# Performance work log

Measured on AMD Instinct MI355X. Metric: run time of the kernel, lower is better.

The kernel has to match this reference:

```python
import jax, jax.numpy as jnp
import numpy as np


def setup_inputs() -> dict:
    key = jax.random.key(0)
    ks = jax.random.split(key, 8)
    B, N = 4, 256
    E, C, H = 64, 128, 256
    return {
        "edge_features": jax.random.normal(ks[0], (B, E, N, N), dtype=jnp.float32),
        "node_features": jax.random.normal(ks[1], (B, C, N), dtype=jnp.float32),
        "W1": jax.random.normal(ks[2], (H, E + 2 * C), dtype=jnp.float32) * 0.05,
        "b1": jax.random.normal(ks[3], (H,), dtype=jnp.float32) * 0.05,
        "W2": jax.random.normal(ks[4], (H, H), dtype=jnp.float32) * 0.05,
        "b2": jax.random.normal(ks[5], (H,), dtype=jnp.float32) * 0.05,
        "W3": jax.random.normal(ks[6], (1, H), dtype=jnp.float32) * 0.05,
        "b3": jax.random.normal(ks[7], (1,), dtype=jnp.float32) * 0.05,
    }


def reference(edge_features, node_features, W1, b1, W2, b2, W3, b3):
    B, C, N = node_features.shape
    # node_addon_row: [B, C, N, N] broadcast along last dim; col along dim 2
    row = jnp.broadcast_to(node_features[:, :, :, None], (B, C, N, N))
    col = jnp.broadcast_to(node_features[:, :, None, :], (B, C, N, N))
    x = jnp.concatenate([edge_features, row, col], axis=1)  # [B, E+2C, N, N]
    # 1x1 conv == channel matmul
    x = jax.nn.relu(jnp.einsum('bcnm,oc->bonm', x, W1) + b1[None, :, None, None])
    x = jax.nn.relu(jnp.einsum('bcnm,oc->bonm', x, W2) + b2[None, :, None, None])
    x = jnp.einsum('bcnm,oc->bonm', x, W3) + b3[None, :, None, None]  # [B,1,N,N]
    return x[:, 0, :, :]
```

## Files before the change

kernel.cpp:

```cpp
#include <hip/hip_runtime.h>
#include <stdint.h>

typedef __bf16 bf16x8 __attribute__((ext_vector_type(8)));
typedef __bf16 bf16x4v __attribute__((ext_vector_type(4)));
typedef float  f32x16 __attribute__((ext_vector_type(16)));
typedef float  f32x4t __attribute__((ext_vector_type(4)));
typedef unsigned int u32x2 __attribute__((ext_vector_type(2)));

#define WS_W1S 0
#define WS_W2S 32768
#define WS_R   163840
#define WS_CT  1212416

__global__ void prep_weights(const float* __restrict__ W1, const float* __restrict__ W2,
                             __bf16* __restrict__ w1s, __bf16* __restrict__ w2s) {
    int t = blockIdx.x * 256 + threadIdx.x;
    int chunk = t >> 6, lane = t & 63;
    if (chunk < 128) {
        int wid = chunk >> 5, ks = (chunk >> 1) & 15, mb = chunk & 1;
        int o = wid * 64 + mb * 32 + (lane & 31);
        int k = ks * 16 + (lane >> 5) * 8;
        const float* src = W2 + o * 256 + k;
        __bf16* dst = w2s + chunk * 512 + lane * 8;
#pragma unroll
        for (int j = 0; j < 8; ++j) dst[j] = (__bf16)src[j];
    } else if (chunk < 160) {
        int c1 = chunk - 128;
        int wid = c1 >> 3, ks = (c1 >> 1) & 3, mb = c1 & 1;
        int o = wid * 64 + mb * 32 + (lane & 31);
        int k = ks * 16 + (lane >> 5) * 8;
        const float* src = W1 + o * 320 + k;
        __bf16* dst = w1s + c1 * 512 + lane * 8;
#pragma unroll
        for (int j = 0; j < 8; ++j) dst[j] = (__bf16)src[j];
    }
}

__global__ __launch_bounds__(256) void prep_rc(
    const float* __restrict__ W1, const float* __restrict__ b1,
    const float* __restrict__ node, float* __restrict__ Rt,
    __bf16* __restrict__ Ctb) {
    __shared__ float nds[128 * 16];
    const int b = blockIdx.x >> 4, j0 = (blockIdx.x & 15) * 16;
    const int o = threadIdx.x;
    {
        int c = threadIdx.x >> 1, jh = (threadIdx.x & 1) * 8;
        const float* src = node + b * 32768 + c * 256 + j0 + jh;
        *(float4*)&nds[c * 16 + jh] = *(const float4*)src;
        *(float4*)&nds[c * 16 + jh + 4] = *(const float4*)(src + 4);
    }
    __syncthreads();
    float aR[16], aC[16];
#pragma unroll
    for (int j = 0; j < 16; ++j) { aR[j] = 0.f; aC[j] = 0.f; }
    const float* wr = W1 + o * 320 + 64;
    const float* wc = W1 + o * 320 + 192;
    for (int c4 = 0; c4 < 32; ++c4) {
        float4 wrv = *(const float4*)(wr + c4 * 4);
        float4 wcv = *(const float4*)(wc + c4 * 4);
        const float* wrp = (const float*)&wrv;
        const float* wcp = (const float*)&wcv;
#pragma unroll
        for (int r = 0; r < 4; ++r) {
            const f32x4t* nrow = (const f32x4t*)&nds[(c4 * 4 + r) * 16];
            f32x4t n0 = nrow[0], n1 = nrow[1], n2 = nrow[2], n3 = nrow[3];
#pragma unroll
            for (int q = 0; q < 4; ++q) {
                aR[q]      = fmaf(wrp[r], n0[q], aR[q]);
                aR[q + 4]  = fmaf(wrp[r], n1[q], aR[q + 4]);
                aR[q + 8]  = fmaf(wrp[r], n2[q], aR[q + 8]);
                aR[q + 12] = fmaf(wrp[r], n3[q], aR[q + 12]);
                aC[q]      = fmaf(wcp[r], n0[q], aC[q]);
                aC[q + 4]  = fmaf(wcp[r], n1[q], aC[q + 4]);
                aC[q + 8]  = fmaf(wcp[r], n2[q], aC[q + 8]);
                aC[q + 12] = fmaf(wcp[r], n3[q], aC[q + 12]);
            }
        }
    }
    float bb = b1[o];
#pragma unroll
    for (int j = 0; j < 16; ++j) {
        int idx = ((b * 256 + j0 + j) << 8) + o;
        Rt[idx] = aR[j] + bb;
        Ctb[idx] = (__bf16)aC[j];
    }
}

__device__ inline void zero_acc(f32x16 acc[2][2]) {
#pragma unroll
    for (int i = 0; i < 2; ++i)
#pragma unroll
        for (int j = 0; j < 2; ++j)
#pragma unroll
            for (int k = 0; k < 16; ++k) acc[i][j][k] = 0.f;
}

__global__ __launch_bounds__(256, 2) void fused_main(
    const float* __restrict__ edge, const __bf16* __restrict__ w1s,
    const __bf16* __restrict__ w2s, const float* __restrict__ Rt,
    const __bf16* __restrict__ Ctb, const float* __restrict__ b2,
    const float* __restrict__ W3, const float* __restrict__ b3,
    float* __restrict__ out) {
    __shared__ unsigned int lds_e[64 * 33];
    __shared__ unsigned int lds_h1[64 * 140];
    __shared__ float lds_p[64 * 9];
    __shared__ float lds_c[512];

    const int tid = threadIdx.x;
    const int wid = tid >> 6;
    const int lane = tid & 63;
    const int p31 = lane & 31;
    const int hi = lane >> 5;
    const int obase = wid * 64;

    const int blk = blockIdx.x;
    const int b   = blk >> 7;
    const int m0  = ((blk >> 5) & 3) << 6;
    const int n0  = (blk & 31) << 3;

    lds_c[tid] = b2[tid];
    lds_c[256 + tid] = W3[tid];

    const float4* eg = (const float4*)edge;
    const int a_ = tid & 15;
    const int epb = tid >> 4;
    float4 pf[4];

#define PREFETCH(nn)                                                        \
    {                                                                       \
        _Pragma("unroll")                                                   \
        for (int r = 0; r < 2; ++r) {                                       \
            int ep = r * 16 + epb;                                          \
            int f4 = (b * 64 + ep * 2) * 16384 + (nn) * 64 + (m0 >> 2) + a_;\
            pf[r * 2]     = eg[f4];                                         \
            pf[r * 2 + 1] = eg[f4 + 16384];                                 \
        }                                                                   \
    }

#define LOAD_Q(bf, q)                                                       \
    {                                                                       \
        _Pragma("unroll")                                                   \
        for (int ksl = 0; ksl < 4; ++ksl)                                   \
            _Pragma("unroll")                                               \
            for (int mb = 0; mb < 2; ++mb)                                  \
                A2q[bf][ksl][mb] = *(const bf16x8*)(w2_s +                  \
                    ((((wid << 4) + (q) * 4 + ksl) << 1) + mb) * 512 + (lane << 3)); \
    }

    PREFETCH(n0);

    bf16x4v CvR[8][2];
#pragma unroll
    for (int mb = 0; mb < 2; ++mb)
#pragma unroll
        for (int rg = 0; rg < 4; ++rg)
#pragma unroll
            for (int nb = 0; nb < 2; ++nb)
                CvR[mb * 4 + rg][nb] = *(const bf16x4v*)(Ctb +
                    ((b * 256 + m0 + nb * 32 + p31) << 8) + obase + mb * 32 + 8 * rg + 4 * hi);

    f32x16 acc[2][2];
    bf16x8 A2q[2][4][2];
    for (int it = 0; it < 8; ++it) {
        const int n = n0 + it;

        uint64_t w1a = (uint64_t)w1s;
        asm volatile("" : "+s"(w1a));
        const __bf16* w1_s = (const __bf16*)w1a;
        uint64_t w2a = (uint64_t)w2s;
        asm volatile("" : "+s"(w2a));
        const __bf16* w2_s = (const __bf16*)w2a;

#pragma unroll
        for (int r = 0; r < 2; ++r) {
            int ep = r * 16 + epb;
            const float* p0 = (const float*)&pf[r * 2];
            const float* p1 = (const float*)&pf[r * 2 + 1];
#pragma unroll
            for (int i = 0; i < 4; ++i) {
                union { __bf16 h[2]; unsigned int u; } t;
                t.h[0] = (__bf16)p0[i];
                t.h[1] = (__bf16)p1[i];
                lds_e[(a_ * 4 + i) * 33 + ep] = t.u;
            }
        }
        bf16x8 A1[2][4];
#pragma unroll
        for (int mb = 0; mb < 2; ++mb)
#pragma unroll
            for (int ks = 0; ks < 4; ++ks)
                A1[mb][ks] = *(const bf16x8*)(w1_s +
                    ((((wid << 2) + ks) << 1) + mb) * 512 + (lane << 3));
        __syncthreads();

        zero_acc(acc);
#pragma unroll
        for (int ks = 0; ks < 4; ++ks) {
            bf16x8 B1[2];
#pragma unroll
            for (int nb = 0; nb < 2; ++nb) {
                union { unsigned int u[4]; bf16x8 v; } bb;
#pragma unroll
                for (int j = 0; j < 4; ++j)
                    bb.u[j] = lds_e[(nb * 32 + p31) * 33 + ks * 8 + hi * 4 + j];
                B1[nb] = bb.v;
            }
#pragma unroll
            for (int mb = 0; mb < 2; ++mb) {
                acc[mb][0] = __builtin_amdgcn_mfma_f32_32x32x16_bf16(A1[mb][ks], B1[0], acc[mb][0], 0, 0, 0);
                acc[mb][1] = __builtin_amdgcn_mfma_f32_32x32x16_bf16(A1[mb][ks], B1[1], acc[mb][1], 0, 0, 0);
            }
        }

        const int nRow = (b * 256 + n) << 8;
#pragma unroll
        for (int mb = 0; mb < 2; ++mb) {
#pragma unroll
            for (int rg = 0; rg < 4; ++rg) {
                int och = obase + mb * 32 + 8 * rg + 4 * hi;
                f32x4t Rv = *(const f32x4t*)(Rt + nRow + och);
#pragma unroll
                for (int nb = 0; nb < 2; ++nb) {
                    int pix = nb * 32 + p31;
                    bf16x4v Cv = CvR[mb * 4 + rg][nb];
                    union { __bf16 h[4]; u32x2 u; } t;
#pragma unroll
                    for (int rr = 0; rr < 4; ++rr) {
                        float v = acc[mb][nb][rg * 4 + rr] + Rv[rr] + (float)Cv[rr];
                        t.h[rr] = (__bf16)fmaxf(v, 0.f);
                    }
                    *(u32x2*)&lds_h1[pix * 140 + (och >> 1)] = t.u;
                }
            }
        }
        LOAD_Q(0, 0);
        if (it < 7) PREFETCH(n + 1);
        __syncthreads();

        zero_acc(acc);
#pragma unroll
        for (int q = 0; q < 4; ++q) {
            if (q < 3) LOAD_Q((q + 1) & 1, q + 1);
#pragma unroll
            for (int ksl = 0; ksl < 4; ++ksl) {
                const int ksg = q * 4 + ksl;
                bf16x8 B2[2];
#pragma unroll
                for (int nb = 0; nb < 2; ++nb)
                    B2[nb] = *(const bf16x8*)&lds_h1[(nb * 32 + p31) * 140 + ksg * 8 + hi * 4];
#pragma unroll
                for (int mb = 0; mb < 2; ++mb) {
                    acc[mb][0] = __builtin_amdgcn_mfma_f32_32x32x16_bf16(A2q[q & 1][ksl][mb], B2[0], acc[mb][0], 0, 0, 0);
                    acc[mb][1] = __builtin_amdgcn_mfma_f32_32x32x16_bf16(A2q[q & 1][ksl][mb], B2[1], acc[mb][1], 0, 0, 0);
                }
            }
        }

        float part0 = 0.f, part1 = 0.f;
#pragma unroll
        for (int mb = 0; mb < 2; ++mb) {
#pragma unroll
            for (int rg = 0; rg < 4; ++rg) {
                int och = obase + mb * 32 + 8 * rg + 4 * hi;
                f32x4t b2v = *(const f32x4t*)&lds_c[och];
                f32x4t w3v = *(const f32x4t*)&lds_c[256 + och];
#pragma unroll
                for (int rr = 0; rr < 4; ++rr) {
                    float h0 = fmaxf(acc[mb][0][rg * 4 + rr] + b2v[rr], 0.f);
                    float h1v = fmaxf(acc[mb][1][rg * 4 + rr] + b2v[rr], 0.f);
                    part0 = fmaf(w3v[rr], h0, part0);
                    part1 = fmaf(w3v[rr], h1v, part1);
                }
            }
        }
        lds_p[(0 * 32 + p31) * 9 + wid * 2 + hi] = part0;
        lds_p[(1 * 32 + p31) * 9 + wid * 2 + hi] = part1;
        __syncthreads();

        if (tid < 64) {
            float s = b3[0];
#pragma unroll
            for (int k = 0; k < 8; ++k) s += lds_p[tid * 9 + k];
            out[((b * 256 + n) << 8) + m0 + tid] = s;
        }
    }
#undef PREFETCH
#undef LOAD_Q
}

extern "C" void kernel_launch(void* const* d_in, const int* in_sizes, int n_in,
                              void* d_out, int out_size, void* d_ws, size_t ws_size,
                              hipStream_t stream) {
    const float* edge = (const float*)d_in[0];
    const float* node = (const float*)d_in[1];
    const float* W1   = (const float*)d_in[2];
    const float* b1   = (const float*)d_in[3];
    const float* W2   = (const float*)d_in[4];
    const float* b2   = (const float*)d_in[5];
    const float* W3   = (const float*)d_in[6];
    const float* b3   = (const float*)d_in[7];
    char* ws = (char*)d_ws;
    __bf16* w1s = (__bf16*)(ws + WS_W1S);
    __bf16* w2s = (__bf16*)(ws + WS_W2S);
    float*  Rt  = (float*)(ws + WS_R);
    __bf16* Ctb = (__bf16*)(ws + WS_CT);

    prep_weights<<<40, 256, 0, stream>>>(W1, W2, w1s, w2s);
    prep_rc<<<64, 256, 0, stream>>>(W1, b1, node, Rt, Ctb);
    fused_main<<<512, 256, 0, stream>>>(edge, w1s, w2s, Rt, Ctb, b2, W3, b3, (float*)d_out);
}
```

Measured before the change: 161.9 us.

## Merge prep kernels, double main grid, raise occupancy, pad LDS, hoist R loads

The two prep kernels are merged into one launch, and the row/col projection is split into finer 4-column blocks so it runs across more workgroups. The main kernel now runs 1024 blocks of 4 rows each instead of 512 blocks of 8, and its launch bounds ask for 3 blocks per CU. The edge LDS tile stride is padded from 33 to 34 so B1 fragments load as 64-bit reads, and the R bias loads are hoisted ahead of the barrier. The cost is a lower register budget per thread, which may cause spills, and the per-block setup is amortised over fewer rows.

```diff
diff --git a/kernel.cpp b/kernel.cpp
--- a/kernel.cpp
+++ b/kernel.cpp
@@ -12,47 +12,44 @@
 #define WS_R   163840
 #define WS_CT  1212416
 
-__global__ void prep_weights(const float* __restrict__ W1, const float* __restrict__ W2,
-                             __bf16* __restrict__ w1s, __bf16* __restrict__ w2s) {
-    int t = blockIdx.x * 256 + threadIdx.x;
-    int chunk = t >> 6, lane = t & 63;
-    if (chunk < 128) {
-        int wid = chunk >> 5, ks = (chunk >> 1) & 15, mb = chunk & 1;
-        int o = wid * 64 + mb * 32 + (lane & 31);
-        int k = ks * 16 + (lane >> 5) * 8;
-        const float* src = W2 + o * 256 + k;
-        __bf16* dst = w2s + chunk * 512 + lane * 8;
-#pragma unroll
-        for (int j = 0; j < 8; ++j) dst[j] = (__bf16)src[j];
-    } else if (chunk < 160) {
-        int c1 = chunk - 128;
-        int wid = c1 >> 3, ks = (c1 >> 1) & 3, mb = c1 & 1;
-        int o = wid * 64 + mb * 32 + (lane & 31);
-        int k = ks * 16 + (lane >> 5) * 8;
-        const float* src = W1 + o * 320 + k;
-        __bf16* dst = w1s + c1 * 512 + lane * 8;
-#pragma unroll
-        for (int j = 0; j < 8; ++j) dst[j] = (__bf16)src[j];
-    }
-}
-
-__global__ __launch_bounds__(256) void prep_rc(
+__global__ __launch_bounds__(256) void prep_all(
     const float* __restrict__ W1, const float* __restrict__ b1,
-    const float* __restrict__ node, float* __restrict__ Rt,
-    __bf16* __restrict__ Ctb) {
-    __shared__ float nds[128 * 16];
-    const int b = blockIdx.x >> 4, j0 = (blockIdx.x & 15) * 16;
+    const float* __restrict__ W2, const float* __restrict__ node,
+    __bf16* __restrict__ w1s, __bf16* __restrict__ w2s,
+    float* __restrict__ Rt, __bf16* __restrict__ Ctb) {
+    __shared__ float nds[128 * 4];
+    const int blk = blockIdx.x;
+    if (blk < 40) {
+        int t = blk * 256 + threadIdx.x;
+        int chunk = t >> 6, lane = t & 63;
+        if (chunk < 128) {
+            int wid = chunk >> 5, ks = (chunk >> 1) & 15, mb = chunk & 1;
+            int o = wid * 64 + mb * 32 + (lane & 31);
+            int k = ks * 16 + (lane >> 5) * 8;
+            const float* src = W2 + o * 256 + k;
+            __bf16* dst = w2s + chunk * 512 + lane * 8;
+#pragma unroll
+            for (int j = 0; j < 8; ++j) dst[j] = (__bf16)src[j];
+        } else if (chunk < 160) {
+            int c1 = chunk - 128;
+            int wid = c1 >> 3, ks = (c1 >> 1) & 3, mb = c1 & 1;
+            int o = wid * 64 + mb * 32 + (lane & 31);
+            int k = ks * 16 + (lane >> 5) * 8;
+            const float* src = W1 + o * 320 + k;
+            __bf16* dst = w1s + c1 * 512 + lane * 8;
+#pragma unroll
+            for (int j = 0; j < 8; ++j) dst[j] = (__bf16)src[j];
+        }
+        return;
+    }
+    const int rcb = blk - 40;
+    const int b = rcb >> 6, j0 = (rcb & 63) << 2;
     const int o = threadIdx.x;
-    {
-        int c = threadIdx.x >> 1, jh = (threadIdx.x & 1) * 8;
-        const float* src = node + b * 32768 + c * 256 + j0 + jh;
-        *(float4*)&nds[c * 16 + jh] = *(const float4*)src;
-        *(float4*)&nds[c * 16 + jh + 4] = *(const float4*)(src + 4);
-    }
+    if (o < 128)
+        *(float4*)&nds[o * 4] = *(const float4*)(node + b * 32768 + o * 256 + j0);
     __syncthreads();
-    float aR[16], aC[16];
-#pragma unroll
-    for (int j = 0; j < 16; ++j) { aR[j] = 0.f; aC[j] = 0.f; }
+    float aR[4] = {0.f, 0.f, 0.f, 0.f};
+    float aC[4] = {0.f, 0.f, 0.f, 0.f};
     const float* wr = W1 + o * 320 + 64;
     const float* wc = W1 + o * 320 + 192;
     for (int c4 = 0; c4 < 32; ++c4) {
@@ -62,24 +59,17 @@
         const float* wcp = (const float*)&wcv;
 #pragma unroll
         for (int r = 0; r < 4; ++r) {
-            const f32x4t* nrow = (const f32x4t*)&nds[(c4 * 4 + r) * 16];
-            f32x4t n0 = nrow[0], n1 = nrow[1], n2 = nrow[2], n3 = nrow[3];
+            f32x4t n4 = *(const f32x4t*)&nds[(c4 * 4 + r) * 4];
 #pragma unroll
             for (int q = 0; q < 4; ++q) {
-                aR[q]      = fmaf(wrp[r], n0[q], aR[q]);
-                aR[q + 4]  = fmaf(wrp[r], n1[q], aR[q + 4]);
-                aR[q + 8]  = fmaf(wrp[r], n2[q], aR[q + 8]);
-                aR[q + 12] = fmaf(wrp[r], n3[q], aR[q + 12]);
-                aC[q]      = fmaf(wcp[r], n0[q], aC[q]);
-                aC[q + 4]  = fmaf(wcp[r], n1[q], aC[q + 4]);
-                aC[q + 8]  = fmaf(wcp[r], n2[q], aC[q + 8]);
-                aC[q + 12] = fmaf(wcp[r], n3[q], aC[q + 12]);
+                aR[q] = fmaf(wrp[r], n4[q], aR[q]);
+                aC[q] = fmaf(wcp[r], n4[q], aC[q]);
             }
         }
     }
     float bb = b1[o];
 #pragma unroll
-    for (int j = 0; j < 16; ++j) {
+    for (int j = 0; j < 4; ++j) {
         int idx = ((b * 256 + j0 + j) << 8) + o;
         Rt[idx] = aR[j] + bb;
         Ctb[idx] = (__bf16)aC[j];
@@ -95,13 +85,13 @@
             for (int k = 0; k < 16; ++k) acc[i][j][k] = 0.f;
 }
 
-__global__ __launch_bounds__(256, 2) void fused_main(
+__global__ __launch_bounds__(256, 3) void fused_main(
     const float* __restrict__ edge, const __bf16* __restrict__ w1s,
     const __bf16* __restrict__ w2s, const float* __restrict__ Rt,
     const __bf16* __restrict__ Ctb, const float* __restrict__ b2,
     const float* __restrict__ W3, const float* __restrict__ b3,
     float* __restrict__ out) {
-    __shared__ unsigned int lds_e[64 * 33];
+    __shared__ unsigned int lds_e[64 * 34];
     __shared__ unsigned int lds_h1[64 * 140];
     __shared__ float lds_p[64 * 9];
     __shared__ float lds_c[512];
@@ -114,9 +104,9 @@
     const int obase = wid * 64;
 
     const int blk = blockIdx.x;
-    const int b   = blk >> 7;
-    const int m0  = ((blk >> 5) & 3) << 6;
-    const int n0  = (blk & 31) << 3;
+    const int b   = blk >> 8;
+    const int m0  = ((blk >> 6) & 3) << 6;
+    const int n0  = (blk & 63) << 2;
 
     lds_c[tid] = b2[tid];
     lds_c[256 + tid] = W3[tid];
@@ -161,7 +151,8 @@
 
     f32x16 acc[2][2];
     bf16x8 A2q[2][4][2];
-    for (int it = 0; it < 8; ++it) {
+#pragma unroll 1
+    for (int it = 0; it < 4; ++it) {
         const int n = n0 + it;
 
         uint64_t w1a = (uint64_t)w1s;
@@ -181,7 +172,7 @@
                 union { __bf16 h[2]; unsigned int u; } t;
                 t.h[0] = (__bf16)p0[i];
                 t.h[1] = (__bf16)p1[i];
-                lds_e[(a_ * 4 + i) * 33 + ep] = t.u;
+                lds_e[(a_ * 4 + i) * 34 + ep] = t.u;
             }
         }
         bf16x8 A1[2][4];
@@ -191,6 +182,13 @@
             for (int ks = 0; ks < 4; ++ks)
                 A1[mb][ks] = *(const bf16x8*)(w1_s +
                     ((((wid << 2) + ks) << 1) + mb) * 512 + (lane << 3));
+        const int nRow = (b * 256 + n) << 8;
+        f32x4t Rv[2][4];
+#pragma unroll
+        for (int mb = 0; mb < 2; ++mb)
+#pragma unroll
+            for (int rg = 0; rg < 4; ++rg)
+                Rv[mb][rg] = *(const f32x4t*)(Rt + nRow + obase + mb * 32 + 8 * rg + 4 * hi);
         __syncthreads();
 
         zero_acc(acc);
@@ -199,10 +197,10 @@
             bf16x8 B1[2];
 #pragma unroll
             for (int nb = 0; nb < 2; ++nb) {
-                union { unsigned int u[4]; bf16x8 v; } bb;
-#pragma unroll
-                for (int j = 0; j < 4; ++j)
-                    bb.u[j] = lds_e[(nb * 32 + p31) * 33 + ks * 8 + hi * 4 + j];
+                union { u32x2 d[2]; bf16x8 v; } bb;
+                const unsigned int* base = &lds_e[(nb * 32 + p31) * 34 + ks * 8 + hi * 4];
+                bb.d[0] = *(const u32x2*)base;
+                bb.d[1] = *(const u32x2*)(base + 2);
                 B1[nb] = bb.v;
             }
 #pragma unroll
@@ -212,13 +210,12 @@
             }
         }
 
-        const int nRow = (b * 256 + n) << 8;
 #pragma unroll
         for (int mb = 0; mb < 2; ++mb) {
 #pragma unroll
             for (int rg = 0; rg < 4; ++rg) {
                 int och = obase + mb * 32 + 8 * rg + 4 * hi;
-                f32x4t Rv = *(const f32x4t*)(Rt + nRow + och);
+                f32x4t Rvv = Rv[mb][rg];
 #pragma unroll
                 for (int nb = 0; nb < 2; ++nb) {
                     int pix = nb * 32 + p31;
@@ -226,7 +223,7 @@
                     union { __bf16 h[4]; u32x2 u; } t;
 #pragma unroll
                     for (int rr = 0; rr < 4; ++rr) {
-                        float v = acc[mb][nb][rg * 4 + rr] + Rv[rr] + (float)Cv[rr];
+                        float v = acc[mb][nb][rg * 4 + rr] + Rvv[rr] + (float)Cv[rr];
                         t.h[rr] = (__bf16)fmaxf(v, 0.f);
                     }
                     *(u32x2*)&lds_h1[pix * 140 + (och >> 1)] = t.u;
@@ -234,7 +231,7 @@
             }
         }
         LOAD_Q(0, 0);
-        if (it < 7) PREFETCH(n + 1);
+        if (it < 3) PREFETCH(n + 1);
         __syncthreads();
 
         zero_acc(acc);
@@ -305,7 +302,6 @@
     float*  Rt  = (float*)(ws + WS_R);
     __bf16* Ctb = (__bf16*)(ws + WS_CT);
 
-    prep_weights<<<40, 256, 0, stream>>>(W1, W2, w1s, w2s);
-    prep_rc<<<64, 256, 0, stream>>>(W1, b1, node, Rt, Ctb);
-    fused_main<<<512, 256, 0, stream>>>(edge, w1s, w2s, Rt, Ctb, b2, W3, b3, (float*)d_out);
+    prep_all<<<296, 256, 0, stream>>>(W1, b1, W2, node, w1s, w2s, Rt, Ctb);
+    fused_main<<<1024, 256, 0, stream>>>(edge, w1s, w2s, Rt, Ctb, b2, W3, b3, (float*)d_out);
 }
```

New measurement: 251.5 us. +55.4%, slower.
